# Kernel tuning notes

Hardware: AMD Instinct MI355X
Metric: run time of the kernel (lower is better)

## Reference

```python
import jax, jax.numpy as jnp
import numpy as np

B, S, E, H = 64, 100, 512, 1024  # H must equal 2*E (bmm in attention)
VS, VT, P = 32000, 32000, 100


def setup_inputs() -> dict:
    key = jax.random.key(0)
    ks = jax.random.split(key, 16)
    sc = 0.02
    return {
        "source_sentences": jax.random.randint(ks[0], (B, S), 0, VS),
        "positions": jax.random.randint(ks[1], (B, S), 0, P),
        "target_words": jax.random.randint(ks[2], (B,), 0, VT),
        "source_lengths": jnp.full((B,), S, dtype=jnp.int64 if jax.config.jax_enable_x64 else jnp.int32),
        "max_len": S,
        "emb_in": jax.random.normal(ks[3], (VS, E), jnp.float32) * sc,
        "emb_out": jax.random.normal(ks[4], (VT, E), jnp.float32) * sc,
        "emb_pos": jax.random.normal(ks[5], (P, E), jnp.float32) * sc,
        "W_scale": jax.random.normal(ks[6], (H, 2 * E), jnp.float32) * sc,
        "b_scale": jnp.zeros((H,), jnp.float32),
        "W_ih": jax.random.normal(ks[7], (H, E + H), jnp.float32) * sc,
        "b_ih": jnp.zeros((H,), jnp.float32),
        "W_hh": jax.random.normal(ks[8], (H, H), jnp.float32) * sc,
        "b_hh": jnp.zeros((H,), jnp.float32),
        "W_proj": jax.random.normal(ks[9], (VT, H), jnp.float32) * sc,
        "b_proj": jnp.zeros((VT,), jnp.float32),
    }


def reference(source_sentences, positions, target_words, source_lengths, max_len,
              emb_in, emb_out, emb_pos, W_scale, b_scale,
              W_ih, b_ih, W_hh, b_hh, W_proj, b_proj):
    # --- encoder_forward ---
    words = emb_in[source_sentences]              # [B,S,E]
    pos = emb_pos[positions]                      # [B,S,E]
    enc = jnp.concatenate([words, pos], axis=-1)  # [B,S,2E] combined embeddings
    h0 = jnp.mean(enc, axis=1) @ W_scale.T + b_scale  # [B,H]
    # --- attention (vectorized form of the per-position bmm loop) ---
    energy = jnp.einsum('bh,bsh->bs', h0, enc)        # [B,S]
    align = jax.nn.softmax(energy, axis=1)            # softmax over source positions
    # original uses torch.mean (not sum) over positions
    context = jnp.mean(align[:, :, None] * enc, axis=1)  # [B,2E] == [B,H]
    # --- decoder step ---
    out_w = emb_out[target_words]                      # [B,E]
    x = jnp.concatenate([out_w, context], axis=-1)     # [B,E+H]
    # nn.RNN single step, tanh nonlinearity
    h = jnp.tanh(x @ W_ih.T + b_ih + h0 @ W_hh.T + b_hh)  # [B,H]
    out = h @ W_proj.T + b_proj                        # [B,VT]
    return (out, h)
```

## Files before the change

kernel.cpp:

```cpp
#include <hip/hip_runtime.h>

typedef __attribute__((ext_vector_type(8))) __bf16 bf16x8;
typedef __attribute__((ext_vector_type(4))) float  f32x4;
typedef unsigned short u16;

__device__ __forceinline__ u16 f2bf(float f) {
    union { float f; unsigned int i; } v; v.f = f;
    unsigned int r = v.i + 0x7fffu + ((v.i >> 16) & 1u);
    return (u16)(r >> 16);
}
__device__ __forceinline__ unsigned pack2(float a, float b) {
    union { float f; unsigned u; } x, y; x.f = a; y.f = b;
    return __builtin_amdgcn_perm(y.u + 0x8000u, x.u + 0x8000u, 0x07060302u);
}

#define B_  64
#define S_  100
#define E_  512
#define H_  1024
#define VT_ 32000
#define Kc  128
#define PITCH 128

__global__ __launch_bounds__(256, 1)
void k1_encmean(const int* __restrict__ src, const int* __restrict__ pos,
                const float* __restrict__ emb_in, const float* __restrict__ emb_pos,
                u16* __restrict__ encmean) {
    int b = blockIdx.x, q4 = blockIdx.y, t = threadIdx.x;
    __shared__ int sidx[S_], pidx[S_];
    __shared__ float part[256][4];
    if (t < S_) { sidx[t] = src[b * S_ + t]; pidx[t] = pos[b * S_ + t]; }
    __syncthreads();

    int f4 = t & 63, g = t >> 6;
    bool isPos = (q4 >= 2);
    const float* base = isPos ? emb_pos : emb_in;
    const int*   idx  = isPos ? pidx : sidx;
    int col = (q4 & 1) * 256 + f4 * 4;

    float a0 = 0.f, a1 = 0.f, a2 = 0.f, a3 = 0.f;
    int s0 = g * 25;
    #pragma unroll 5
    for (int s = s0; s < s0 + 25; s++) {
        const float4 v = *(const float4*)(base + (size_t)idx[s] * E_ + col);
        a0 += v.x; a1 += v.y; a2 += v.z; a3 += v.w;
    }
    part[t][0] = a0; part[t][1] = a1; part[t][2] = a2; part[t][3] = a3;
    __syncthreads();

    if (t < 64) {
        const float inv = 1.0f / (float)S_;
        float r0 = 0.f, r1 = 0.f, r2 = 0.f, r3 = 0.f;
        #pragma unroll
        for (int g2 = 0; g2 < 4; g2++) {
            r0 += part[g2 * 64 + t][0]; r1 += part[g2 * 64 + t][1];
            r2 += part[g2 * 64 + t][2]; r3 += part[g2 * 64 + t][3];
        }
        int e = q4 * 256 + t * 4;
        u16* o = encmean + (size_t)b * (2 * E_) + e;
        o[0] = f2bf(r0 * inv); o[1] = f2bf(r1 * inv);
        o[2] = f2bf(r2 * inv); o[3] = f2bf(r3 * inv);
    }
}

#define MFMA16(a, bfrag, c) __builtin_amdgcn_mfma_f32_16x16x32_bf16((a), (bfrag), (c), 0, 0, 0)

template<int KTOT>
__device__ __forceinline__ void gemm_lds(const u16* __restrict__ A,
                                         const float* __restrict__ W,
                                         int jt, u16* __restrict__ ldsW,
                                         f32x4 acc[4], int t) {
    constexpr int NC = KTOT / Kc;
    const int lane = t & 63, w = t >> 6, m = lane & 15, q = lane >> 4;
    const int r = t >> 2, c4 = t & 3;
    const float* wsrc = W + (size_t)(jt + r) * KTOT + c4 * 4;
    const u16*   arow = A + (size_t)(w * 16 + m) * KTOT + q * 8;
    const int halfoff = (c4 & 1) * 4;

    float4 v[8];
    #pragma unroll
    for (int i = 0; i < 8; i++) v[i] = *(const float4*)(wsrc + i * 16);
    #pragma unroll
    for (int i = 0; i < 8; i++) {
        int U = (c4 >> 1) + 2 * i;
        uint2 p; p.x = pack2(v[i].x, v[i].y); p.y = pack2(v[i].z, v[i].w);
        *(uint2*)(ldsW + r * PITCH + ((U ^ (r & 15)) * 8) + halfoff) = p;
    }
    __syncthreads();

    for (int c = 0; c < NC; c++) {
        if (c + 1 < NC) {
            #pragma unroll
            for (int i = 0; i < 8; i++)
                v[i] = *(const float4*)(wsrc + (c + 1) * Kc + i * 16);
        }
        const u16* lb = ldsW + (c & 1) * (64 * PITCH);
        const u16* ar = arow + c * Kc;
        #pragma unroll
        for (int ks = 0; ks < 4; ks++) {
            bf16x8 a = *(const bf16x8*)(ar + ks * 32);
            #pragma unroll
            for (int f = 0; f < 4; f++) {
                int rr = f * 16 + m;
                int U  = ks * 4 + q;
                bf16x8 bfr = *(const bf16x8*)(lb + rr * PITCH + ((U ^ (rr & 15)) * 8));
                acc[f] = MFMA16(a, bfr, acc[f]);
            }
        }
        if (c + 1 < NC) {
            u16* wd = ldsW + ((c + 1) & 1) * (64 * PITCH) + r * PITCH;
            #pragma unroll
            for (int i = 0; i < 8; i++) {
                int U = (c4 >> 1) + 2 * i;
                uint2 p; p.x = pack2(v[i].x, v[i].y); p.y = pack2(v[i].z, v[i].w);
                *(uint2*)(wd + ((U ^ (r & 15)) * 8) + halfoff) = p;
            }
        }
        __syncthreads();
    }
}

__global__ __launch_bounds__(256, 1)
void k2_h0(const u16* __restrict__ encmean, const float* __restrict__ Wscale,
           const float* __restrict__ bscale,
           float* __restrict__ h0f, u16* __restrict__ h0b) {
    __shared__ u16 ldsW[2 * 64 * PITCH];
    int t = threadIdx.x, lane = t & 63, w = t >> 6, m = lane & 15, q = lane >> 4;
    int jt = blockIdx.x * 64;
    f32x4 acc[4] = {{0,0,0,0},{0,0,0,0},{0,0,0,0},{0,0,0,0}};
    gemm_lds<2 * E_>(encmean, Wscale, jt, ldsW, acc, t);
    #pragma unroll
    for (int f = 0; f < 4; f++) {
        int j = jt + 16 * f + m;
        float bias = bscale[j];
        #pragma unroll
        for (int r = 0; r < 4; r++) {
            int b = w * 16 + q * 4 + r;
            float vv = acc[f][r] + bias;
            h0f[(size_t)b * H_ + j] = vv;
            h0b[(size_t)b * H_ + j] = f2bf(vv);
        }
    }
}

__global__ __launch_bounds__(256, 1)
void k3_attn(const int* __restrict__ src, const int* __restrict__ pos,
             const int* __restrict__ tgt,
             const float* __restrict__ emb_in, const float* __restrict__ emb_pos,
             const float* __restrict__ emb_out,
             const float* __restrict__ h0f, u16* __restrict__ x) {
    int b = blockIdx.x, t = threadIdx.x;
    __shared__ float h0s[2 * E_];
    __shared__ int sidx[S_], pidx[S_];
    __shared__ float energy[S_];
    __shared__ float align_s[S_];

    for (int i = t; i < 2 * E_; i += 256) h0s[i] = h0f[(size_t)b * H_ + i];
    if (t < S_) { sidx[t] = src[b * S_ + t]; pidx[t] = pos[b * S_ + t]; }
    __syncthreads();

    int lane = t & 63, w = t >> 6;
    for (int s = w; s < S_; s += 4) {
        const float* ri = emb_in  + (size_t)sidx[s] * E_;
        const float* rp = emb_pos + (size_t)pidx[s] * E_;
        float acc = 0.f;
        #pragma unroll
        for (int ii = 0; ii < 8; ii++) { int k = lane + 64 * ii; acc += ri[k] * h0s[k]; }
        #pragma unroll
        for (int ii = 0; ii < 8; ii++) { int k = lane + 64 * ii; acc += rp[k] * h0s[E_ + k]; }
        #pragma unroll
        for (int off = 32; off; off >>= 1) acc += __shfl_down(acc, off);
        if (lane == 0) energy[s] = acc;
    }
    __syncthreads();

    if (t < 64) {
        float e0 = energy[t];
        float e1 = (t + 64 < S_) ? energy[t + 64] : -1e30f;
        float mx = fmaxf(e0, e1);
        #pragma unroll
        for (int off = 32; off; off >>= 1) mx = fmaxf(mx, __shfl_xor(mx, off));
        float p0 = expf(e0 - mx);
        float p1 = (t + 64 < S_) ? expf(e1 - mx) : 0.f;
        float ss = p0 + p1;
        #pragma unroll
        for (int off = 32; off; off >>= 1) ss += __shfl_xor(ss, off);
        float inv = 1.0f / (ss * (float)S_);
        align_s[t] = p0 * inv;
        if (t + 64 < S_) align_s[t + 64] = p1 * inv;
    }
    __syncthreads();

    if (t < 128) {
        int o = t;
        bool isPos = (o >= 64);
        const float* base = isPos ? emb_pos : emb_in;
        const int* idx  = isPos ? pidx : sidx;
        int eo = (o & 63) * 8;
        float c[8] = {0,0,0,0,0,0,0,0};
        for (int s = 0; s < S_; s++) {
            const float* row = base + (size_t)idx[s] * E_ + eo;
            float al = align_s[s];
            const float4 v0 = *(const float4*)(row);
            const float4 v1 = *(const float4*)(row + 4);
            c[0] += al * v0.x; c[1] += al * v0.y; c[2] += al * v0.z; c[3] += al * v0.w;
            c[4] += al * v1.x; c[5] += al * v1.y; c[6] += al * v1.z; c[7] += al * v1.w;
        }
        u16* xo = x + (size_t)b * (E_ + H_) + E_ + o * 8;
        #pragma unroll
        for (int i = 0; i < 8; i++) xo[i] = f2bf(c[i]);
    } else {
        int i = t - 128;
        int tw = tgt[b];
        const float4 v = *((const float4*)(emb_out + (size_t)tw * E_) + i);
        ushort4 o; o.x = f2bf(v.x); o.y = f2bf(v.y); o.z = f2bf(v.z); o.w = f2bf(v.w);
        *((ushort4*)(x + (size_t)b * (E_ + H_)) + i) = o;
    }
}

__global__ __launch_bounds__(256, 1)
void k4_h(const u16* __restrict__ xb, const float* __restrict__ Wih,
          const float* __restrict__ bih,
          const u16* __restrict__ h0b, const float* __restrict__ Whh,
          const float* __restrict__ bhh,
          float* __restrict__ houtf, u16* __restrict__ hbf) {
    __shared__ u16 ldsW[2 * 64 * PITCH];
    int t = threadIdx.x, lane = t & 63, w = t >> 6, m = lane & 15, q = lane >> 4;
    int jt = blockIdx.x * 64;
    f32x4 acc[4] = {{0,0,0,0},{0,0,0,0},{0,0,0,0},{0,0,0,0}};
    gemm_lds<E_ + H_>(xb,  Wih, jt, ldsW, acc, t);
    gemm_lds<H_>     (h0b, Whh, jt, ldsW, acc, t);
    #pragma unroll
    for (int f = 0; f < 4; f++) {
        int j = jt + 16 * f + m;
        float bias = bih[j] + bhh[j];
        #pragma unroll
        for (int r = 0; r < 4; r++) {
            int b = w * 16 + q * 4 + r;
            float vv = tanhf(acc[f][r] + bias);
            houtf[(size_t)b * H_ + j] = vv;
            hbf[(size_t)b * H_ + j] = f2bf(vv);
        }
    }
}

__global__ __launch_bounds__(256, 1)
void k5_out(const u16* __restrict__ hb, const float* __restrict__ Wp,
            const float* __restrict__ bp, float* __restrict__ out) {
    __shared__ u16 ldsW[2 * 64 * PITCH];
    int t = threadIdx.x, lane = t & 63, w = t >> 6, m = lane & 15, q = lane >> 4;
    int jt = blockIdx.x * 64;
    f32x4 acc[4] = {{0,0,0,0},{0,0,0,0},{0,0,0,0},{0,0,0,0}};
    gemm_lds<H_>(hb, Wp, jt, ldsW, acc, t);
    #pragma unroll
    for (int f = 0; f < 4; f++) {
        int j = jt + 16 * f + m;
        float bias = bp[j];
        #pragma unroll
        for (int r = 0; r < 4; r++) {
            int b = w * 16 + q * 4 + r;
            out[(size_t)b * VT_ + j] = acc[f][r] + bias;
        }
    }
}

extern "C" void kernel_launch(void* const* d_in, const int* in_sizes, int n_in,
                              void* d_out, int out_size, void* d_ws, size_t ws_size,
                              hipStream_t stream) {
    const int*   src     = (const int*)d_in[0];
    const int*   pos     = (const int*)d_in[1];
    const int*   tgt     = (const int*)d_in[2];
    const float* emb_in  = (const float*)d_in[5];
    const float* emb_out = (const float*)d_in[6];
    const float* emb_pos = (const float*)d_in[7];
    const float* Wscale  = (const float*)d_in[8];
    const float* bscale  = (const float*)d_in[9];
    const float* Wih     = (const float*)d_in[10];
    const float* bih     = (const float*)d_in[11];
    const float* Whh     = (const float*)d_in[12];
    const float* bhh     = (const float*)d_in[13];
    const float* Wproj   = (const float*)d_in[14];
    const float* bproj   = (const float*)d_in[15];

    char* ws = (char*)d_ws;
    u16*   encmean = (u16*)(ws);
    float* h0f     = (float*)(ws + 131072);
    u16*   h0b     = (u16*)(ws + 393216);
    u16*   xb      = (u16*)(ws + 524288);
    u16*   hbf     = (u16*)(ws + 720896);

    float* out   = (float*)d_out;
    float* houtf = out + (size_t)B_ * VT_;

    hipLaunchKernelGGL(k1_encmean, dim3(B_, 4),     dim3(256), 0, stream,
                       src, pos, emb_in, emb_pos, encmean);
    hipLaunchKernelGGL(k2_h0,      dim3(H_ / 64),   dim3(256), 0, stream,
                       encmean, Wscale, bscale, h0f, h0b);
    hipLaunchKernelGGL(k3_attn,    dim3(B_),        dim3(256), 0, stream,
                       src, pos, tgt, emb_in, emb_pos, emb_out, h0f, xb);
    hipLaunchKernelGGL(k4_h,       dim3(H_ / 64),   dim3(256), 0, stream,
                       xb, Wih, bih, h0b, Whh, bhh, houtf, hbf);
    hipLaunchKernelGGL(k5_out,     dim3(VT_ / 64),  dim3(256), 0, stream,
                       hbf, Wproj, bproj, out);
}
```

Before: 365.9 us.

## Split-K the h0 and RNN GEMMs across more blocks with separate reductions

The h0 GEMM is split four ways along K and the RNN-step GEMMs ten ways, which raises the grids from 16 blocks to 64 and 160 so more CUs stream the weights. Partial sums go to workspace buffers. The attention kernel reduces the h0 partials and adds the bias, and a new kernel reduces the RNN partials and applies tanh. Launch bounds also move to 2 blocks per CU. The cost is extra partial-sum traffic and one more kernel launch.

After: 322.0 us. 1.14x faster.

```diff
diff --git a/kernel.cpp b/kernel.cpp
--- a/kernel.cpp
+++ b/kernel.cpp
@@ -65,16 +65,16 @@
 
 #define MFMA16(a, bfrag, c) __builtin_amdgcn_mfma_f32_16x16x32_bf16((a), (bfrag), (c), 0, 0, 0)
 
-template<int KTOT>
+template<int KLEN, int LDA, int LDW>
 __device__ __forceinline__ void gemm_lds(const u16* __restrict__ A,
                                          const float* __restrict__ W,
-                                         int jt, u16* __restrict__ ldsW,
+                                         int jt, int koff, u16* __restrict__ ldsW,
                                          f32x4 acc[4], int t) {
-    constexpr int NC = KTOT / Kc;
+    constexpr int NC = KLEN / Kc;
     const int lane = t & 63, w = t >> 6, m = lane & 15, q = lane >> 4;
     const int r = t >> 2, c4 = t & 3;
-    const float* wsrc = W + (size_t)(jt + r) * KTOT + c4 * 4;
-    const u16*   arow = A + (size_t)(w * 16 + m) * KTOT + q * 8;
+    const float* wsrc = W + (size_t)(jt + r) * LDW + koff + c4 * 4;
+    const u16*   arow = A + (size_t)(w * 16 + m) * LDA + koff + q * 8;
     const int halfoff = (c4 & 1) * 4;
 
     float4 v[8];
@@ -120,25 +120,21 @@
     }
 }
 
-__global__ __launch_bounds__(256, 1)
-void k2_h0(const u16* __restrict__ encmean, const float* __restrict__ Wscale,
-           const float* __restrict__ bscale,
-           float* __restrict__ h0f, u16* __restrict__ h0b) {
+__global__ __launch_bounds__(256, 2)
+void k2_h0p(const u16* __restrict__ encmean, const float* __restrict__ Wscale,
+            float* __restrict__ part2) {
     __shared__ u16 ldsW[2 * 64 * PITCH];
     int t = threadIdx.x, lane = t & 63, w = t >> 6, m = lane & 15, q = lane >> 4;
-    int jt = blockIdx.x * 64;
+    int jt = blockIdx.x * 64, sp = blockIdx.y;
     f32x4 acc[4] = {{0,0,0,0},{0,0,0,0},{0,0,0,0},{0,0,0,0}};
-    gemm_lds<2 * E_>(encmean, Wscale, jt, ldsW, acc, t);
+    gemm_lds<256, 2 * E_, 2 * E_>(encmean, Wscale, jt, sp * 256, ldsW, acc, t);
     #pragma unroll
     for (int f = 0; f < 4; f++) {
         int j = jt + 16 * f + m;
-        float bias = bscale[j];
-        #pragma unroll
-        for (int r = 0; r < 4; r++) {
-            int b = w * 16 + q * 4 + r;
-            float vv = acc[f][r] + bias;
-            h0f[(size_t)b * H_ + j] = vv;
-            h0b[(size_t)b * H_ + j] = f2bf(vv);
+        #pragma unroll
+        for (int r2 = 0; r2 < 4; r2++) {
+            int bb = w * 16 + q * 4 + r2;
+            part2[(size_t)(sp * B_ + bb) * H_ + j] = acc[f][r2];
         }
     }
 }
@@ -148,14 +144,21 @@
              const int* __restrict__ tgt,
              const float* __restrict__ emb_in, const float* __restrict__ emb_pos,
              const float* __restrict__ emb_out,
-             const float* __restrict__ h0f, u16* __restrict__ x) {
+             const float* __restrict__ part2, const float* __restrict__ bscale,
+             u16* __restrict__ x, u16* __restrict__ h0b) {
     int b = blockIdx.x, t = threadIdx.x;
     __shared__ float h0s[2 * E_];
     __shared__ int sidx[S_], pidx[S_];
     __shared__ float energy[S_];
     __shared__ float align_s[S_];
 
-    for (int i = t; i < 2 * E_; i += 256) h0s[i] = h0f[(size_t)b * H_ + i];
+    for (int i = t; i < 2 * E_; i += 256) {
+        float v = bscale[i];
+        #pragma unroll
+        for (int ks = 0; ks < 4; ks++) v += part2[(size_t)(ks * B_ + b) * H_ + i];
+        h0s[i] = v;
+        h0b[(size_t)b * H_ + i] = f2bf(v);
+    }
     if (t < S_) { sidx[t] = src[b * S_ + t]; pidx[t] = pos[b * S_ + t]; }
     __syncthreads();
 
@@ -218,40 +221,55 @@
     }
 }
 
-__global__ __launch_bounds__(256, 1)
-void k4_h(const u16* __restrict__ xb, const float* __restrict__ Wih,
-          const float* __restrict__ bih,
-          const u16* __restrict__ h0b, const float* __restrict__ Whh,
-          const float* __restrict__ bhh,
-          float* __restrict__ houtf, u16* __restrict__ hbf) {
+__global__ __launch_bounds__(256, 2)
+void k4_hp(const u16* __restrict__ xb, const float* __restrict__ Wih,
+           const u16* __restrict__ h0b, const float* __restrict__ Whh,
+           float* __restrict__ part4) {
     __shared__ u16 ldsW[2 * 64 * PITCH];
     int t = threadIdx.x, lane = t & 63, w = t >> 6, m = lane & 15, q = lane >> 4;
-    int jt = blockIdx.x * 64;
+    int jt = blockIdx.x * 64, sp = blockIdx.y;
     f32x4 acc[4] = {{0,0,0,0},{0,0,0,0},{0,0,0,0},{0,0,0,0}};
-    gemm_lds<E_ + H_>(xb,  Wih, jt, ldsW, acc, t);
-    gemm_lds<H_>     (h0b, Whh, jt, ldsW, acc, t);
+    if (sp < 6) gemm_lds<256, E_ + H_, E_ + H_>(xb,  Wih, jt, sp * 256,       ldsW, acc, t);
+    else        gemm_lds<256, H_,      H_     >(h0b, Whh, jt, (sp - 6) * 256, ldsW, acc, t);
     #pragma unroll
     for (int f = 0; f < 4; f++) {
         int j = jt + 16 * f + m;
-        float bias = bih[j] + bhh[j];
-        #pragma unroll
-        for (int r = 0; r < 4; r++) {
-            int b = w * 16 + q * 4 + r;
-            float vv = tanhf(acc[f][r] + bias);
-            houtf[(size_t)b * H_ + j] = vv;
-            hbf[(size_t)b * H_ + j] = f2bf(vv);
+        #pragma unroll
+        for (int r2 = 0; r2 < 4; r2++) {
+            int bb = w * 16 + q * 4 + r2;
+            part4[(size_t)(sp * B_ + bb) * H_ + j] = acc[f][r2];
         }
     }
 }
 
 __global__ __launch_bounds__(256, 1)
+void k4_red(const float* __restrict__ part4,
+            const float* __restrict__ bih, const float* __restrict__ bhh,
+            float* __restrict__ houtf, u16* __restrict__ hbf) {
+    int b = blockIdx.x, t = threadIdx.x;
+    int j = t * 4;
+    float4 s  = *(const float4*)(bih + j);
+    const float4 b2 = *(const float4*)(bhh + j);
+    s.x += b2.x; s.y += b2.y; s.z += b2.z; s.w += b2.w;
+    #pragma unroll
+    for (int ks = 0; ks < 10; ks++) {
+        const float4 p = *(const float4*)(part4 + (size_t)(ks * B_ + b) * H_ + j);
+        s.x += p.x; s.y += p.y; s.z += p.z; s.w += p.w;
+    }
+    float4 h; h.x = tanhf(s.x); h.y = tanhf(s.y); h.z = tanhf(s.z); h.w = tanhf(s.w);
+    *(float4*)(houtf + (size_t)b * H_ + j) = h;
+    ushort4 o; o.x = f2bf(h.x); o.y = f2bf(h.y); o.z = f2bf(h.z); o.w = f2bf(h.w);
+    *(ushort4*)(hbf + (size_t)b * H_ + j) = o;
+}
+
+__global__ __launch_bounds__(256, 2)
 void k5_out(const u16* __restrict__ hb, const float* __restrict__ Wp,
             const float* __restrict__ bp, float* __restrict__ out) {
     __shared__ u16 ldsW[2 * 64 * PITCH];
     int t = threadIdx.x, lane = t & 63, w = t >> 6, m = lane & 15, q = lane >> 4;
     int jt = blockIdx.x * 64;
     f32x4 acc[4] = {{0,0,0,0},{0,0,0,0},{0,0,0,0},{0,0,0,0}};
-    gemm_lds<H_>(hb, Wp, jt, ldsW, acc, t);
+    gemm_lds<H_, H_, H_>(hb, Wp, jt, 0, ldsW, acc, t);
     #pragma unroll
     for (int f = 0; f < 4; f++) {
         int j = jt + 16 * f + m;
@@ -284,22 +302,25 @@
 
     char* ws = (char*)d_ws;
     u16*   encmean = (u16*)(ws);
-    float* h0f     = (float*)(ws + 131072);
-    u16*   h0b     = (u16*)(ws + 393216);
-    u16*   xb      = (u16*)(ws + 524288);
-    u16*   hbf     = (u16*)(ws + 720896);
+    u16*   xb      = (u16*)(ws + 131072);
+    u16*   h0b     = (u16*)(ws + 327680);
+    u16*   hbf     = (u16*)(ws + 458752);
+    float* part2   = (float*)(ws + 589824);
+    float* part4   = (float*)(ws + 1638400);
 
     float* out   = (float*)d_out;
     float* houtf = out + (size_t)B_ * VT_;
 
-    hipLaunchKernelGGL(k1_encmean, dim3(B_, 4),     dim3(256), 0, stream,
+    hipLaunchKernelGGL(k1_encmean, dim3(B_, 4),      dim3(256), 0, stream,
                        src, pos, emb_in, emb_pos, encmean);
-    hipLaunchKernelGGL(k2_h0,      dim3(H_ / 64),   dim3(256), 0, stream,
-                       encmean, Wscale, bscale, h0f, h0b);
-    hipLaunchKernelGGL(k3_attn,    dim3(B_),        dim3(256), 0, stream,
-                       src, pos, tgt, emb_in, emb_pos, emb_out, h0f, xb);
-    hipLaunchKernelGGL(k4_h,       dim3(H_ / 64),   dim3(256), 0, stream,
-                       xb, Wih, bih, h0b, Whh, bhh, houtf, hbf);
-    hipLaunchKernelGGL(k5_out,     dim3(VT_ / 64),  dim3(256), 0, stream,
+    hipLaunchKernelGGL(k2_h0p,     dim3(H_ / 64, 4), dim3(256), 0, stream,
+                       encmean, Wscale, part2);
+    hipLaunchKernelGGL(k3_attn,    dim3(B_),         dim3(256), 0, stream,
+                       src, pos, tgt, emb_in, emb_pos, emb_out, part2, bscale, xb, h0b);
+    hipLaunchKernelGGL(k4_hp,      dim3(H_ / 64, 10), dim3(256), 0, stream,
+                       xb, Wih, h0b, Whh, part4);
+    hipLaunchKernelGGL(k4_red,     dim3(B_),         dim3(256), 0, stream,
+                       part4, bih, bhh, houtf, hbf);
+    hipLaunchKernelGGL(k5_out,     dim3(VT_ / 64),   dim3(256), 0, stream,
                        hbf, Wproj, bproj, out);
 }
```
